# Performance work log

Measured on AMD Instinct MI355X. Metric: run time of the kernel, lower is better.

Reference implementation:

```python
import jax, jax.numpy as jnp
import numpy as np

B, T, E, H = 2, 2048, 1024, 16
D = E // H  # head dim = 64


def setup_inputs() -> dict:
    key = jax.random.key(0)
    kx, kq, kk, kv, kw = jax.random.split(key, 5)
    # kaiming-normal-like init for per-head projections, xavier-like for output proj
    qkv_std = (2.0 / E) ** 0.5
    w_std = (6.0 / (E + E)) ** 0.5 / (3.0 ** 0.5)
    x = jax.random.normal(kx, (B, T, E), dtype=jnp.float32)
    Wq = jax.random.normal(kq, (H, E, D), dtype=jnp.float32) * qkv_std
    Wk = jax.random.normal(kk, (H, E, D), dtype=jnp.float32) * qkv_std
    Wv = jax.random.normal(kv, (H, E, D), dtype=jnp.float32) * qkv_std
    Wo = jax.random.normal(kw, (E, E), dtype=jnp.float32) * w_std
    return {"x": x, "Wq": Wq, "Wk": Wk, "Wv": Wv, "Wo": Wo}


def reference(x, Wq, Wk, Wv, Wo):
    # per-head projections, batched over heads: bte,hed->bhtd
    q = jnp.einsum('bte,hed->bhtd', x, Wq)
    k = jnp.einsum('bte,hed->bhtd', x, Wk)
    v = jnp.einsum('bte,hed->bhtd', x, Wv)
    scale = 1.0 / jnp.sqrt(jnp.asarray(D, dtype=q.dtype))
    scores = jnp.einsum('bhtd,bhTd->bhtT', q, k) * scale  # [B,H,T,T]
    attn = jax.nn.softmax(scores, axis=-1)
    heads = jnp.einsum('bhtT,bhTd->bhtd', attn, v)  # [B,H,T,D]
    # concat heads along feature dim (head order preserved)
    combined = heads.transpose(0, 2, 1, 3).reshape(B, T, E)
    return combined @ Wo + x
```

## Files before the change

### kernel.cpp

```cpp
#include <hip/hip_runtime.h>
#include <hip/hip_bf16.h>


#define B_ 2
#define T_ 2048
#define E_ 1024
#define H_ 16
#define D_ 64
#define VTS_ 2176
#define LD_ 72

typedef _Float16 h8 __attribute__((ext_vector_type(8)));
typedef _Float16 h4 __attribute__((ext_vector_type(4)));
typedef float f32x4 __attribute__((ext_vector_type(4)));

union U4 { uint4 u; h8 h; };

__device__ __forceinline__ float h2f(unsigned short s) {
  _Float16 h;
  __builtin_memcpy(&h, &s, 2);
  return (float)h;
}

__device__ __forceinline__ unsigned short f2h(float f) {
  _Float16 h = (_Float16)f;
  unsigned short s;
  __builtin_memcpy(&s, &h, 2);
  return s;
}

__global__ __launch_bounds__(256) void cvt_x(const float* __restrict__ x,
                                             unsigned short* __restrict__ xh) {
  const size_t i = ((size_t)blockIdx.x * 256 + threadIdx.x) * 4;
  const float4 f = *(const float4*)(x + i);
  ushort4 pk;
  pk.x = f2h(f.x); pk.y = f2h(f.y); pk.z = f2h(f.z); pk.w = f2h(f.w);
  *(ushort4*)(xh + i) = pk;
}

__global__ __launch_bounds__(256) void tconv_w(
    const float* __restrict__ Wq, const float* __restrict__ Wk,
    const float* __restrict__ Wv, unsigned short* __restrict__ wt) {
  __shared__ float ts[64][65];
  const int p = blockIdx.z, h = blockIdx.y;
  const float* src = ((p == 0) ? Wq : (p == 1) ? Wk : Wv) + (size_t)h * E_ * D_;
  unsigned short* dst = wt + (size_t)(p * H_ + h) * D_ * E_;
  const int r0 = blockIdx.x * 64;
  const int lr = threadIdx.x >> 4, lc = (threadIdx.x & 15) * 4;
#pragma unroll
  for (int it = 0; it < 4; it++) {
    const float4 f = *(const float4*)(src + (size_t)(r0 + lr + it * 16) * D_ + lc);
    ts[lr + it * 16][lc] = f.x; ts[lr + it * 16][lc + 1] = f.y;
    ts[lr + it * 16][lc + 2] = f.z; ts[lr + it * 16][lc + 3] = f.w;
  }
  __syncthreads();
#pragma unroll
  for (int it = 0; it < 4; it++) {
    const int dr = lr + it * 16;
    ushort4 pk;
    pk.x = f2h(ts[lc + 0][dr]); pk.y = f2h(ts[lc + 1][dr]);
    pk.z = f2h(ts[lc + 2][dr]); pk.w = f2h(ts[lc + 3][dr]);
    *(ushort4*)(dst + (size_t)dr * E_ + r0 + lc) = pk;
  }
}

__global__ __launch_bounds__(256) void tconv_wo(const float* __restrict__ Wo,
                                                unsigned short* __restrict__ wot) {
  __shared__ float ts[64][65];
  const int r0 = blockIdx.x * 64;
  const int c0 = blockIdx.y * 64;
  const int lr = threadIdx.x >> 4, lc = (threadIdx.x & 15) * 4;
#pragma unroll
  for (int it = 0; it < 4; it++) {
    const float4 f = *(const float4*)(Wo + (size_t)(r0 + lr + it * 16) * E_ + c0 + lc);
    ts[lr + it * 16][lc] = f.x; ts[lr + it * 16][lc + 1] = f.y;
    ts[lr + it * 16][lc + 2] = f.z; ts[lr + it * 16][lc + 3] = f.w;
  }
  __syncthreads();
#pragma unroll
  for (int it = 0; it < 4; it++) {
    const int dr = lr + it * 16;
    ushort4 pk;
    pk.x = f2h(ts[lc + 0][dr]); pk.y = f2h(ts[lc + 1][dr]);
    pk.z = f2h(ts[lc + 2][dr]); pk.w = f2h(ts[lc + 3][dr]);
    *(ushort4*)(wot + (size_t)(c0 + dr) * E_ + r0 + lc) = pk;
  }
}

__global__ __launch_bounds__(256) void qkv_mfma(
    const unsigned short* __restrict__ xh, const unsigned short* __restrict__ wt,
    unsigned short* __restrict__ qo, unsigned short* __restrict__ ko,
    unsigned short* __restrict__ vo)
{
  __shared__ unsigned short xs[128 * LD_];
  __shared__ unsigned short wsb[64 * LD_];
  __shared__ unsigned short Cl[4][32 * 72];

  const int tid = threadIdx.x;
  const int w = tid >> 6, lane = tid & 63;
  const int m16 = lane & 15, quad = lane >> 4;
  const int h = blockIdx.y, p = blockIdx.z;
  const int n0 = blockIdx.x * 128;
  const unsigned short* wb = wt + (size_t)(p * H_ + h) * D_ * E_;

  const int sr = tid >> 3;
  const int sc = (tid & 7) * 8;

  f32x4 acc[2][4];
#pragma unroll
  for (int rt = 0; rt < 2; rt++)
#pragma unroll
    for (int ct = 0; ct < 4; ct++) acc[rt][ct] = (f32x4){0.f, 0.f, 0.f, 0.f};

  for (int e0 = 0; e0 < E_; e0 += 64) {
    __syncthreads();
#pragma unroll
    for (int it = 0; it < 4; it++) {
      const int row = it * 32 + sr;
      *(uint4*)(xs + row * LD_ + sc) =
          *(const uint4*)(xh + (size_t)(n0 + row) * E_ + e0 + sc);
    }
#pragma unroll
    for (int it = 0; it < 2; it++) {
      const int row = it * 32 + sr;
      *(uint4*)(wsb + row * LD_ + sc) =
          *(const uint4*)(wb + (size_t)row * E_ + e0 + sc);
    }
    __syncthreads();

#pragma unroll
    for (int kk = 0; kk < 64; kk += 32) {
      U4 a0, a1, bf[4];
      a0.u = *(const uint4*)(xs + (w * 32 + m16) * LD_ + kk + quad * 8);
      a1.u = *(const uint4*)(xs + (w * 32 + 16 + m16) * LD_ + kk + quad * 8);
#pragma unroll
      for (int ct = 0; ct < 4; ct++)
        bf[ct].u = *(const uint4*)(wsb + (ct * 16 + m16) * LD_ + kk + quad * 8);
#pragma unroll
      for (int ct = 0; ct < 4; ct++) {
        acc[0][ct] = __builtin_amdgcn_mfma_f32_16x16x32_f16(a0.h, bf[ct].h, acc[0][ct], 0, 0, 0);
        acc[1][ct] = __builtin_amdgcn_mfma_f32_16x16x32_f16(a1.h, bf[ct].h, acc[1][ct], 0, 0, 0);
      }
    }
  }

  const int nw = n0 + w * 32;
  const int b  = n0 >> 11;
  const int t0 = nw & (T_ - 1);
  const size_t bh = (size_t)(b * H_ + h);

  if (p == 2) {
#pragma unroll
    for (int rt = 0; rt < 2; rt++)
#pragma unroll
      for (int ct = 0; ct < 4; ct++) {
        const int d = ct * 16 + m16;
        const int t = t0 + rt * 16 + quad * 4;
        ushort4 pk;
        pk.x = f2h(acc[rt][ct][0]); pk.y = f2h(acc[rt][ct][1]);
        pk.z = f2h(acc[rt][ct][2]); pk.w = f2h(acc[rt][ct][3]);
        *(ushort4*)(vo + (bh * D_ + d) * (size_t)VTS_ + t) = pk;
      }
  } else {
    unsigned short* outp = (p == 0) ? qo : ko;
    unsigned short* Cw = &Cl[w][0];
#pragma unroll
    for (int rt = 0; rt < 2; rt++)
#pragma unroll
      for (int ct = 0; ct < 4; ct++)
#pragma unroll
        for (int r = 0; r < 4; r++)
          Cw[(rt * 16 + quad * 4 + r) * 72 + ct * 16 + m16] = f2h(acc[rt][ct][r]);
    const int row = lane >> 1;
    const int half = (lane & 1) * 32;
    const uint4 d0 = *(const uint4*)(Cw + row * 72 + half);
    const uint4 d1 = *(const uint4*)(Cw + row * 72 + half + 8);
    const uint4 d2 = *(const uint4*)(Cw + row * 72 + half + 16);
    const uint4 d3 = *(const uint4*)(Cw + row * 72 + half + 24);
    unsigned short* dst = outp + (bh * T_ + t0 + row) * D_ + half;
    *(uint4*)(dst)      = d0;
    *(uint4*)(dst + 8)  = d1;
    *(uint4*)(dst + 16) = d2;
    *(uint4*)(dst + 24) = d3;
  }
}

__global__ __launch_bounds__(256) void attn_kernel(
    const unsigned short* __restrict__ q, const unsigned short* __restrict__ k,
    const unsigned short* __restrict__ vt, unsigned short* __restrict__ comb)
{
  __shared__ unsigned short Kt[2][64 * LD_];
  __shared__ unsigned short Vt[2][64 * LD_];

  const int tid  = threadIdx.x;
  const int w    = tid >> 6;
  const int lane = tid & 63;
  const int m16  = lane & 15;
  const int quad = lane >> 4;

  const int flat = blockIdx.x;
  const int swz  = (flat & 7) * 128 + (flat >> 3);
  const int xq   = swz & 31;
  const int h    = (swz >> 5) & 15;
  const int b    = swz >> 9;

  const size_t bh = (size_t)(b * H_ + h);
  const int q0 = xq * 64 + w * 16;

  U4 aQ0, aQ1;
  {
    const unsigned short* qrow = q + (bh * T_ + q0 + m16) * (size_t)D_;
    aQ0.u = *(const uint4*)(qrow + quad * 8);
    aQ1.u = *(const uint4*)(qrow + 32 + quad * 8);
    aQ0.h = aQ0.h * (_Float16)0.125f;
    aQ1.h = aQ1.h * (_Float16)0.125f;
  }

  f32x4 o[4];
#pragma unroll
  for (int i = 0; i < 4; i++) o[i] = (f32x4){0.f, 0.f, 0.f, 0.f};
  float mrow = -1e30f;
  float lrow = 0.f;

  const unsigned short* kb  = k  + bh * (size_t)(T_ * D_);
  const unsigned short* vtb = vt + bh * (size_t)(D_ * VTS_);

  const int sr = tid >> 3;
  const int sc = (tid & 7) * 8;

  uint4 kr0, kr1, vr0, vr1;
  kr0 = *(const uint4*)(kb + (size_t)sr * D_ + sc);
  kr1 = *(const uint4*)(kb + (size_t)(32 + sr) * D_ + sc);
  vr0 = *(const uint4*)(vtb + (size_t)sr * VTS_ + sc);
  vr1 = *(const uint4*)(vtb + (size_t)(32 + sr) * VTS_ + sc);
  *(uint4*)(&Kt[0][0] + sr * LD_ + sc)        = kr0;
  *(uint4*)(&Kt[0][0] + (32 + sr) * LD_ + sc) = kr1;
  *(uint4*)(&Vt[0][0] + sr * LD_ + sc)        = vr0;
  *(uint4*)(&Vt[0][0] + (32 + sr) * LD_ + sc) = vr1;
  __syncthreads();

  const int NT = T_ / 64;
  for (int t = 0; t < NT; t++) {
    const int cur = t & 1;
    const unsigned short* Kc = &Kt[cur][0];
    const unsigned short* Vc = &Vt[cur][0];
    const bool more = (t + 1 < NT);
    if (more) {
      const int kt = (t + 1) * 64;
      kr0 = *(const uint4*)(kb + (size_t)(kt + sr) * D_ + sc);
      kr1 = *(const uint4*)(kb + (size_t)(kt + 32 + sr) * D_ + sc);
      vr0 = *(const uint4*)(vtb + (size_t)sr * VTS_ + kt + sc);
      vr1 = *(const uint4*)(vtb + (size_t)(32 + sr) * VTS_ + kt + sc);
    }

    f32x4 st[4];
#pragma unroll
    for (int ct = 0; ct < 4; ct++) {
      U4 kf0, kf1;
      kf0.u = *(const uint4*)(Kc + (ct * 16 + m16) * LD_ + quad * 8);
      kf1.u = *(const uint4*)(Kc + (ct * 16 + m16) * LD_ + 32 + quad * 8);
      f32x4 z = {0.f, 0.f, 0.f, 0.f};
      z = __builtin_amdgcn_mfma_f32_16x16x32_f16(kf0.h, aQ0.h, z, 0, 0, 0);
      z = __builtin_amdgcn_mfma_f32_16x16x32_f16(kf1.h, aQ1.h, z, 0, 0, 0);
      st[ct] = z;
    }

    const float m0 = fmaxf(fmaxf(st[0][0], st[0][1]), fmaxf(st[0][2], st[0][3]));
    const float m1 = fmaxf(fmaxf(st[1][0], st[1][1]), fmaxf(st[1][2], st[1][3]));
    const float m2 = fmaxf(fmaxf(st[2][0], st[2][1]), fmaxf(st[2][2], st[2][3]));
    const float m3 = fmaxf(fmaxf(st[3][0], st[3][1]), fmaxf(st[3][2], st[3][3]));
    float ml = fmaxf(fmaxf(m0, m1), fmaxf(m2, m3));
    ml = fmaxf(ml, __shfl_xor(ml, 16));
    ml = fmaxf(ml, __shfl_xor(ml, 32));

    if (!__all(ml - mrow <= 8.0f)) {
      const float mn2 = fmaxf(mrow, ml);
      const float a   = __expf(mrow - mn2);
      float al[4];
#pragma unroll
      for (int r = 0; r < 4; r++) al[r] = __shfl(a, quad * 4 + r);
#pragma unroll
      for (int i = 0; i < 4; i++)
#pragma unroll
        for (int r = 0; r < 4; r++) o[i][r] *= al[r];
      lrow *= a;
      mrow = mn2;
    }
    const float mn = mrow;

    float sl = 0.f;
    h4 pf[4];
#pragma unroll
    for (int ct = 0; ct < 4; ct++) {
      const float e0 = __expf(st[ct][0] - mn);
      const float e1 = __expf(st[ct][1] - mn);
      const float e2 = __expf(st[ct][2] - mn);
      const float e3 = __expf(st[ct][3] - mn);
      sl += (e0 + e1) + (e2 + e3);
      pf[ct] = (h4){(_Float16)e0, (_Float16)e1, (_Float16)e2, (_Float16)e3};
    }
    sl += __shfl_xor(sl, 16);
    sl += __shfl_xor(sl, 32);
    lrow += sl;

#pragma unroll
    for (int ctd = 0; ctd < 4; ctd++) {
      const unsigned short* vrow = Vc + (ctd * 16 + m16) * LD_ + quad * 4;
#pragma unroll
      for (int ctk = 0; ctk < 4; ctk++) {
        const h4 vf = *(const h4*)(vrow + ctk * 16);
        o[ctd] = __builtin_amdgcn_mfma_f32_16x16x16f16(pf[ctk], vf, o[ctd], 0, 0, 0);
      }
    }

    if (more) {
      __syncthreads();
      unsigned short* Kn = &Kt[cur ^ 1][0];
      unsigned short* Vn = &Vt[cur ^ 1][0];
      *(uint4*)(Kn + sr * LD_ + sc)        = kr0;
      *(uint4*)(Kn + (32 + sr) * LD_ + sc) = kr1;
      *(uint4*)(Vn + sr * LD_ + sc)        = vr0;
      *(uint4*)(Vn + (32 + sr) * LD_ + sc) = vr1;
      __syncthreads();
    }
  }

  float linv[4];
#pragma unroll
  for (int r = 0; r < 4; r++) linv[r] = 1.f / __shfl(lrow, quad * 4 + r);

#pragma unroll
  for (int r = 0; r < 4; r++) {
    const int tq = q0 + quad * 4 + r;
    unsigned short* dst = comb + ((size_t)b * T_ + tq) * E_ + h * D_;
    dst[m16]      = f2h(o[0][r] * linv[r]);
    dst[16 + m16] = f2h(o[1][r] * linv[r]);
    dst[32 + m16] = f2h(o[2][r] * linv[r]);
    dst[48 + m16] = f2h(o[3][r] * linv[r]);
  }
}

__global__ __launch_bounds__(256) void out_mfma(
    const unsigned short* __restrict__ comb, const unsigned short* __restrict__ wot,
    const float* __restrict__ x, float* __restrict__ out)
{
  __shared__ unsigned short cs[128 * LD_];
  __shared__ unsigned short wsb[64 * LD_];

  const int tid = threadIdx.x;
  const int w = tid >> 6, lane = tid & 63;
  const int m16 = lane & 15, quad = lane >> 4;
  const int n0 = blockIdx.x * 128;
  const int j0 = blockIdx.y * 64;

  const int sr = tid >> 3;
  const int sc = (tid & 7) * 8;

  f32x4 acc[2][4];
#pragma unroll
  for (int rt = 0; rt < 2; rt++)
#pragma unroll
    for (int ct = 0; ct < 4; ct++) acc[rt][ct] = (f32x4){0.f, 0.f, 0.f, 0.f};

  for (int e0 = 0; e0 < E_; e0 += 64) {
    __syncthreads();
#pragma unroll
    for (int it = 0; it < 4; it++) {
      const int row = it * 32 + sr;
      *(uint4*)(cs + row * LD_ + sc) =
          *(const uint4*)(comb + (size_t)(n0 + row) * E_ + e0 + sc);
    }
#pragma unroll
    for (int it = 0; it < 2; it++) {
      const int row = it * 32 + sr;
      *(uint4*)(wsb + row * LD_ + sc) =
          *(const uint4*)(wot + (size_t)(j0 + row) * E_ + e0 + sc);
    }
    __syncthreads();

#pragma unroll
    for (int kk = 0; kk < 64; kk += 32) {
      U4 a0, a1, bf[4];
      a0.u = *(const uint4*)(cs + (w * 32 + m16) * LD_ + kk + quad * 8);
      a1.u = *(const uint4*)(cs + (w * 32 + 16 + m16) * LD_ + kk + quad * 8);
#pragma unroll
      for (int ct = 0; ct < 4; ct++)
        bf[ct].u = *(const uint4*)(wsb + (ct * 16 + m16) * LD_ + kk + quad * 8);
#pragma unroll
      for (int ct = 0; ct < 4; ct++) {
        acc[0][ct] = __builtin_amdgcn_mfma_f32_16x16x32_f16(a0.h, bf[ct].h, acc[0][ct], 0, 0, 0);
        acc[1][ct] = __builtin_amdgcn_mfma_f32_16x16x32_f16(a1.h, bf[ct].h, acc[1][ct], 0, 0, 0);
      }
    }
  }

  const int nw = n0 + w * 32;
#pragma unroll
  for (int rt = 0; rt < 2; rt++)
#pragma unroll
    for (int r = 0; r < 4; r++) {
      const int n = nw + rt * 16 + quad * 4 + r;
      const float* xr = x + (size_t)n * E_ + j0;
      float* orow = out + (size_t)n * E_ + j0;
#pragma unroll
      for (int ct = 0; ct < 4; ct++) {
        const int j = ct * 16 + m16;
        orow[j] = acc[rt][ct][r] + xr[j];
      }
    }
}

extern "C" void kernel_launch(void* const* d_in, const int* in_sizes, int n_in,
                              void* d_out, int out_size, void* d_ws, size_t ws_size,
                              hipStream_t stream) {
  (void)in_sizes; (void)n_in; (void)out_size; (void)ws_size;

  const float* x  = (const float*)d_in[0];
  const float* Wq = (const float*)d_in[1];
  const float* Wk = (const float*)d_in[2];
  const float* Wv = (const float*)d_in[3];
  const float* Wo = (const float*)d_in[4];
  float* out = (float*)d_out;

  unsigned short* ws0  = (unsigned short*)d_ws;
  unsigned short* xh   = ws0;
  unsigned short* wt   = ws0 + 4194304;
  unsigned short* wot  = ws0 + 7340032;
  unsigned short* qh   = ws0 + 8388608;
  unsigned short* kh   = ws0 + 12582912;
  unsigned short* vth  = ws0 + 16777216;
  unsigned short* comb = xh;

  cvt_x<<<dim3(B_ * T_ * E_ / 1024), dim3(256), 0, stream>>>(x, xh);
  tconv_w<<<dim3(E_ / 64, H_, 3), dim3(256), 0, stream>>>(Wq, Wk, Wv, wt);
  tconv_wo<<<dim3(E_ / 64, E_ / 64), dim3(256), 0, stream>>>(Wo, wot);

  qkv_mfma<<<dim3(B_ * T_ / 128, H_, 3), dim3(256), 0, stream>>>(xh, wt, qh, kh, vth);

  attn_kernel<<<dim3(B_ * H_ * (T_ / 64)), dim3(256), 0, stream>>>(qh, kh, vth, comb);

  out_mfma<<<dim3(B_ * T_ / 128, E_ / 64), dim3(256), 0, stream>>>(comb, wot, x, out);
}
```

Baseline: 221.4 us.

## Use 128-query attention blocks, fold scale into Wq, switch softmax to exp2

New measurement: 206.3 us. 1.07x faster.

```diff
diff --git a/kernel.cpp b/kernel.cpp
--- a/kernel.cpp
+++ b/kernel.cpp
@@ -15,6 +15,7 @@
 typedef float f32x4 __attribute__((ext_vector_type(4)));
 
 union U4 { uint4 u; h8 h; };
+union V8 { uint4 u; h4 f[2]; };
 
 __device__ __forceinline__ float h2f(unsigned short s) {
   _Float16 h;
@@ -27,6 +28,14 @@
   unsigned short s;
   __builtin_memcpy(&s, &h, 2);
   return s;
+}
+
+__device__ __forceinline__ float fexp2(float x) {
+#if __has_builtin(__builtin_amdgcn_exp2f)
+  return __builtin_amdgcn_exp2f(x);
+#else
+  return __expf(x * 0.6931471805599453f);
+#endif
 }
 
 __global__ __launch_bounds__(256) void cvt_x(const float* __restrict__ x,
@@ -45,13 +54,14 @@
   const int p = blockIdx.z, h = blockIdx.y;
   const float* src = ((p == 0) ? Wq : (p == 1) ? Wk : Wv) + (size_t)h * E_ * D_;
   unsigned short* dst = wt + (size_t)(p * H_ + h) * D_ * E_;
+  const float scl = (p == 0) ? 0.18033688011112042f : 1.0f;
   const int r0 = blockIdx.x * 64;
   const int lr = threadIdx.x >> 4, lc = (threadIdx.x & 15) * 4;
 #pragma unroll
   for (int it = 0; it < 4; it++) {
     const float4 f = *(const float4*)(src + (size_t)(r0 + lr + it * 16) * D_ + lc);
-    ts[lr + it * 16][lc] = f.x; ts[lr + it * 16][lc + 1] = f.y;
-    ts[lr + it * 16][lc + 2] = f.z; ts[lr + it * 16][lc + 3] = f.w;
+    ts[lr + it * 16][lc] = f.x * scl; ts[lr + it * 16][lc + 1] = f.y * scl;
+    ts[lr + it * 16][lc + 2] = f.z * scl; ts[lr + it * 16][lc + 3] = f.w * scl;
   }
   __syncthreads();
 #pragma unroll
@@ -185,7 +195,7 @@
   }
 }
 
-__global__ __launch_bounds__(256) void attn_kernel(
+__global__ __launch_bounds__(512) void attn_kernel(
     const unsigned short* __restrict__ q, const unsigned short* __restrict__ k,
     const unsigned short* __restrict__ vt, unsigned short* __restrict__ comb)
 {
@@ -199,21 +209,19 @@
   const int quad = lane >> 4;
 
   const int flat = blockIdx.x;
-  const int swz  = (flat & 7) * 128 + (flat >> 3);
-  const int xq   = swz & 31;
-  const int h    = (swz >> 5) & 15;
-  const int b    = swz >> 9;
+  const int swz  = (flat & 7) * 64 + (flat >> 3);
+  const int xq   = swz & 15;
+  const int h    = (swz >> 4) & 15;
+  const int b    = swz >> 8;
 
   const size_t bh = (size_t)(b * H_ + h);
-  const int q0 = xq * 64 + w * 16;
+  const int q0 = xq * 128 + w * 16;
 
   U4 aQ0, aQ1;
   {
     const unsigned short* qrow = q + (bh * T_ + q0 + m16) * (size_t)D_;
     aQ0.u = *(const uint4*)(qrow + quad * 8);
     aQ1.u = *(const uint4*)(qrow + 32 + quad * 8);
-    aQ0.h = aQ0.h * (_Float16)0.125f;
-    aQ1.h = aQ1.h * (_Float16)0.125f;
   }
 
   f32x4 o[4];
@@ -222,21 +230,24 @@
   float mrow = -1e30f;
   float lrow = 0.f;
 
-  const unsigned short* kb  = k  + bh * (size_t)(T_ * D_);
-  const unsigned short* vtb = vt + bh * (size_t)(D_ * VTS_);
-
   const int sr = tid >> 3;
   const int sc = (tid & 7) * 8;
-
-  uint4 kr0, kr1, vr0, vr1;
-  kr0 = *(const uint4*)(kb + (size_t)sr * D_ + sc);
-  kr1 = *(const uint4*)(kb + (size_t)(32 + sr) * D_ + sc);
-  vr0 = *(const uint4*)(vtb + (size_t)sr * VTS_ + sc);
-  vr1 = *(const uint4*)(vtb + (size_t)(32 + sr) * VTS_ + sc);
-  *(uint4*)(&Kt[0][0] + sr * LD_ + sc)        = kr0;
-  *(uint4*)(&Kt[0][0] + (32 + sr) * LD_ + sc) = kr1;
-  *(uint4*)(&Vt[0][0] + sr * LD_ + sc)        = vr0;
-  *(uint4*)(&Vt[0][0] + (32 + sr) * LD_ + sc) = vr1;
+  const int vdoff = ((sc >> 2) & 3) * 16 + (sc >> 4) * 4;
+
+  const unsigned short* kp = k  + bh * (size_t)(T_ * D_)   + (size_t)sr * D_ + sc;
+  const unsigned short* vp = vt + bh * (size_t)(D_ * VTS_) + (size_t)sr * VTS_ + sc;
+
+  uint4 kr, vr;
+  kr = *(const uint4*)(kp);
+  vr = *(const uint4*)(vp);
+  kp += 64 * D_; vp += 64;
+  {
+    unsigned short* kd = &Kt[0][0] + sr * LD_ + sc;
+    unsigned short* vd = &Vt[0][0] + sr * LD_ + vdoff;
+    *(uint4*)(kd) = kr;
+    *(uint2*)(vd)      = make_uint2(vr.x, vr.y);
+    *(uint2*)(vd + 16) = make_uint2(vr.z, vr.w);
+  }
   __syncthreads();
 
   const int NT = T_ / 64;
@@ -246,11 +257,9 @@
     const unsigned short* Vc = &Vt[cur][0];
     const bool more = (t + 1 < NT);
     if (more) {
-      const int kt = (t + 1) * 64;
-      kr0 = *(const uint4*)(kb + (size_t)(kt + sr) * D_ + sc);
-      kr1 = *(const uint4*)(kb + (size_t)(kt + 32 + sr) * D_ + sc);
-      vr0 = *(const uint4*)(vtb + (size_t)sr * VTS_ + kt + sc);
-      vr1 = *(const uint4*)(vtb + (size_t)(32 + sr) * VTS_ + kt + sc);
+      kr = *(const uint4*)(kp);
+      vr = *(const uint4*)(vp);
+      kp += 64 * D_; vp += 64;
     }
 
     f32x4 st[4];
@@ -273,9 +282,9 @@
     ml = fmaxf(ml, __shfl_xor(ml, 16));
     ml = fmaxf(ml, __shfl_xor(ml, 32));
 
-    if (!__all(ml - mrow <= 8.0f)) {
+    if (!__all(ml - mrow <= 11.0f)) {
       const float mn2 = fmaxf(mrow, ml);
-      const float a   = __expf(mrow - mn2);
+      const float a   = fexp2(mrow - mn2);
       float al[4];
 #pragma unroll
       for (int r = 0; r < 4; r++) al[r] = __shfl(a, quad * 4 + r);
@@ -292,10 +301,10 @@
     h4 pf[4];
 #pragma unroll
     for (int ct = 0; ct < 4; ct++) {
-      const float e0 = __expf(st[ct][0] - mn);
-      const float e1 = __expf(st[ct][1] - mn);
-      const float e2 = __expf(st[ct][2] - mn);
-      const float e3 = __expf(st[ct][3] - mn);
+      const float e0 = fexp2(st[ct][0] - mn);
+      const float e1 = fexp2(st[ct][1] - mn);
+      const float e2 = fexp2(st[ct][2] - mn);
+      const float e3 = fexp2(st[ct][3] - mn);
       sl += (e0 + e1) + (e2 + e3);
       pf[ct] = (h4){(_Float16)e0, (_Float16)e1, (_Float16)e2, (_Float16)e3};
     }
@@ -305,22 +314,23 @@
 
 #pragma unroll
     for (int ctd = 0; ctd < 4; ctd++) {
-      const unsigned short* vrow = Vc + (ctd * 16 + m16) * LD_ + quad * 4;
-#pragma unroll
-      for (int ctk = 0; ctk < 4; ctk++) {
-        const h4 vf = *(const h4*)(vrow + ctk * 16);
-        o[ctd] = __builtin_amdgcn_mfma_f32_16x16x16f16(pf[ctk], vf, o[ctd], 0, 0, 0);
-      }
+      const unsigned short* vrow = Vc + (ctd * 16 + m16) * LD_ + quad * 16;
+      V8 va, vb;
+      va.u = *(const uint4*)(vrow);
+      vb.u = *(const uint4*)(vrow + 8);
+      o[ctd] = __builtin_amdgcn_mfma_f32_16x16x16f16(pf[0], va.f[0], o[ctd], 0, 0, 0);
+      o[ctd] = __builtin_amdgcn_mfma_f32_16x16x16f16(pf[1], va.f[1], o[ctd], 0, 0, 0);
+      o[ctd] = __builtin_amdgcn_mfma_f32_16x16x16f16(pf[2], vb.f[0], o[ctd], 0, 0, 0);
+      o[ctd] = __builtin_amdgcn_mfma_f32_16x16x16f16(pf[3], vb.f[1], o[ctd], 0, 0, 0);
     }
 
     if (more) {
       __syncthreads();
-      unsigned short* Kn = &Kt[cur ^ 1][0];
-      unsigned short* Vn = &Vt[cur ^ 1][0];
-      *(uint4*)(Kn + sr * LD_ + sc)        = kr0;
-      *(uint4*)(Kn + (32 + sr) * LD_ + sc) = kr1;
-      *(uint4*)(Vn + sr * LD_ + sc)        = vr0;
-      *(uint4*)(Vn + (32 + sr) * LD_ + sc) = vr1;
+      unsigned short* kd = &Kt[cur ^ 1][0] + sr * LD_ + sc;
+      unsigned short* vd = &Vt[cur ^ 1][0] + sr * LD_ + vdoff;
+      *(uint4*)(kd) = kr;
+      *(uint2*)(vd)      = make_uint2(vr.x, vr.y);
+      *(uint2*)(vd + 16) = make_uint2(vr.z, vr.w);
       __syncthreads();
     }
   }
@@ -437,7 +447,7 @@
 
   qkv_mfma<<<dim3(B_ * T_ / 128, H_, 3), dim3(256), 0, stream>>>(xh, wt, qh, kh, vth);
 
-  attn_kernel<<<dim3(B_ * H_ * (T_ / 64)), dim3(256), 0, stream>>>(qh, kh, vth, comb);
+  attn_kernel<<<dim3(B_ * H_ * (T_ / 128)), dim3(512), 0, stream>>>(qh, kh, vth, comb);
 
   out_mfma<<<dim3(B_ * T_ / 128, E_ / 64), dim3(256), 0, stream>>>(comb, wot, x, out);
 }
```
